# Kernel tuning notes

Hardware: AMD Instinct MI355X
Metric: run time of the kernel (lower is better)

The kernel has to match this reference:

```python
import jax, jax.numpy as jnp
import numpy as np
from jax import lax

B, C_IN, T = 256, 1, 1632
HID, CB_DIM, NUM_TOK, NUM_Q = 64, 512, 1024, 2


def conv_k2s2(x, W, b):
    # Conv1d(kernel=2, stride=2): x [B,Ci,T] -> [B,Co,T//2]; W [Co,Ci,2]
    Bx, Ci, Tx = x.shape
    xr = x.reshape(Bx, Ci, Tx // 2, 2)
    return jnp.einsum('bitk,oik->bot', xr, W) + b[None, :, None]


def convT_k2s2(x, W, b):
    # ConvTranspose1d(kernel=2, stride=2): x [B,Ci,T] -> [B,Co,2T]; W [Ci,Co,2] (torch layout)
    Bx, Ci, Tx = x.shape
    y = jnp.einsum('bit,iok->botk', x, W)  # [B,Co,T,2]
    Co = W.shape[1]
    return y.reshape(Bx, Co, 2 * Tx) + b[None, :, None]


def conv1x1(x, W, b):
    # W [Co,Ci]
    return jnp.einsum('bit,oi->bot', x, W) + b[None, :, None]


def residual_vq(x, codebooks):
    # x [B,t,D]; codebooks [NUM_Q, NUM_TOK, D]. Euclidean argmin + straight-through.
    residual = x
    quantized_out = jnp.zeros_like(x)
    all_idx, all_loss = [], []
    for q in range(codebooks.shape[0]):
        cb = codebooks[q]  # [N,D]
        # squared euclidean distance, single large GEMM
        d2 = (jnp.sum(residual ** 2, -1, keepdims=True)
              - 2.0 * jnp.einsum('btd,nd->btn', residual, cb)
              + jnp.sum(cb ** 2, -1))  # [B,t,N]
        idx = jnp.argmin(d2, axis=-1)  # [B,t]
        quant = cb[idx]  # gather [B,t,D]
        # commitment loss (codebook treated as fixed / EMA-updated)
        loss = jnp.mean((lax.stop_gradient(quant) - residual) ** 2)
        # straight-through estimator
        quant_st = residual + lax.stop_gradient(quant - residual)
        residual = residual - lax.stop_gradient(quant)
        quantized_out = quantized_out + quant_st
        all_idx.append(idx)
        all_loss.append(loss)
    return quantized_out, jnp.stack(all_idx, -1), jnp.stack(all_loss)


def setup_inputs() -> dict:
    key = jax.random.key(0)
    ks = jax.random.split(key, 16)
    s = 0.02
    return {
        'img': jax.random.normal(ks[0], (B, C_IN, T), jnp.float32),
        'W_e1': jax.random.normal(ks[1], (HID, C_IN, 2), jnp.float32) * s,
        'b_e1': jnp.zeros((HID,), jnp.float32),
        'W_e2': jax.random.normal(ks[2], (HID, HID, 2), jnp.float32) * s,
        'b_e2': jnp.zeros((HID,), jnp.float32),
        'W_e3': jax.random.normal(ks[3], (CB_DIM, HID), jnp.float32) * s,
        'b_e3': jnp.zeros((CB_DIM,), jnp.float32),
        'codebooks': jax.random.normal(ks[4], (NUM_Q, NUM_TOK, CB_DIM), jnp.float32),
        'Wt_d1': jax.random.normal(ks[5], (CB_DIM, HID, 2), jnp.float32) * s,
        'b_d1': jnp.zeros((HID,), jnp.float32),
        'Wt_d2': jax.random.normal(ks[6], (HID, HID, 2), jnp.float32) * s,
        'b_d2': jnp.zeros((HID,), jnp.float32),
        'W_d3': jax.random.normal(ks[7], (C_IN, HID), jnp.float32) * s,
        'b_d3': jnp.zeros((C_IN,), jnp.float32),
    }


def reference(img, W_e1, b_e1, W_e2, b_e2, W_e3, b_e3, codebooks,
              Wt_d1, b_d1, Wt_d2, b_d2, W_d3, b_d3):
    # encoder
    h = jax.nn.relu(conv_k2s2(img, W_e1, b_e1))
    h = jax.nn.relu(conv_k2s2(h, W_e2, b_e2))
    encoded = conv1x1(h, W_e3, b_e3)  # [B,512,408]
    # residual VQ over tokens
    x = jnp.transpose(encoded, (0, 2, 1))  # b c t -> b t c
    quantized, indices, commit_loss = residual_vq(x, codebooks)
    quantized = jnp.transpose(quantized, (0, 2, 1))  # b t c -> b c t
    # decoder
    d = jax.nn.relu(convT_k2s2(quantized, Wt_d1, b_d1))
    d = jax.nn.relu(convT_k2s2(d, Wt_d2, b_d2))
    out = conv1x1(d, W_d3, b_d3)  # [B,1,1632]
    recon_loss = jnp.mean((img - out) ** 2)
    return out, recon_loss, commit_loss, indices, quantized
```

## Files before the change

### kernel.cpp

```cpp
#include <hip/hip_runtime.h>

#define NB    256
#define TLEN  1632
#define HIDC  64
#define CBD   512
#define NTOK  1024
#define T2L   816
#define T4L   408
#define MTOK  (NB*T4L)
#define M2TOK (NB*T2L)
#define MOUT  (NB*TLEN)

#define DO_OUT    ((size_t)0)
#define DO_RECON  ((size_t)417792)
#define DO_IDX    ((size_t)417795)
#define DO_QUANT  ((size_t)626691)
#define DO_XRH    ((size_t)417796)
#define DO_R1H    (DO_XRH + (size_t)MTOK*256)

typedef unsigned short u16;
typedef unsigned long long u64;
typedef __attribute__((ext_vector_type(8))) short short8;
typedef __attribute__((ext_vector_type(4))) float f32x4;
typedef __attribute__((ext_vector_type(8))) _Float16 half8;
typedef __attribute__((ext_vector_type(4))) _Float16 half4;

static constexpr size_t OFF_XR  = 0;
static constexpr size_t OFF_H1  = OFF_XR + (size_t)MTOK*512;
static constexpr size_t OFF_H2  = OFF_H1 + (size_t)NB*T2L*64;
static constexpr size_t OFF_BE2 = OFF_H2 + (size_t)NB*T4L*64;
static constexpr size_t OFF_BD1 = OFF_BE2 + 8192;
static constexpr size_t OFF_BD2 = OFF_BD1 + 65536;
static constexpr size_t OFF_BX1 = OFF_BD2 + 8192;
static constexpr size_t OFF_BX2 = OFF_BX1 + 128;
static constexpr size_t OFF_ZB  = OFF_BX2 + 128;
static constexpr size_t OFF_C2  = OFF_ZB + 128;
static constexpr size_t OFF_SLOT= OFF_C2 + 2048;
static constexpr size_t OFF_IDXI= OFF_SLOT + 1536;
static constexpr size_t OFF_KEYS= OFF_IDXI + (size_t)MTOK*2;
static constexpr size_t OFF_FC  = OFF_KEYS + (size_t)MTOK*4;
static constexpr size_t OFF_FLAG= OFF_FC + 4;
static constexpr size_t OFF_CBH = OFF_FLAG + (size_t)MTOK*2;
static constexpr size_t OFF_CBL = OFF_CBH + 524288;
static constexpr size_t OFF_P0  = OFF_CBL + 524288;
static constexpr size_t OFF_P1  = OFF_P0 + 131072;
static constexpr size_t OFF_PAIRS = OFF_P1 + 131072;

__device__ inline u64 shfl_xor_u64_w16(u64 v, int m) {
    unsigned lo = (unsigned)v, hi = (unsigned)(v >> 32);
    lo = __shfl_xor(lo, m, 16);
    hi = __shfl_xor(hi, m, 16);
    return (((u64)hi) << 32) | lo;
}
__device__ inline u64 packkey(float d, int n) {
    unsigned u = __float_as_uint(d);
    u = (u & 0x80000000u) ? ~u : (u | 0x80000000u);
    return (((u64)u) << 32) | (unsigned)n;
}
__device__ inline float unpackd(u64 k) {
    unsigned u = (unsigned)(k >> 32);
    u = (u & 0x80000000u) ? (u & 0x7fffffffu) : ~u;
    return __uint_as_float(u);
}
__device__ inline void merge2(u64& k1, u64& k2, u64 o1, u64 o2) {
    u64 n1 = (k1 < o1) ? k1 : o1;
    u64 hi = (k1 < o1) ? o1 : k1;
    u64 cand = (k1 <= o1) ? k2 : o2;
    u64 n2 = (hi < cand) ? hi : cand;
    k1 = n1; k2 = n2;
}
__device__ inline half4 cvt_h4(float4 v) {
    half4 h;
    h.x = (_Float16)v.x; h.y = (_Float16)v.y;
    h.z = (_Float16)v.z; h.w = (_Float16)v.w;
    return h;
}
__device__ inline void gll16(const u16* g, u16* l) {
    __builtin_amdgcn_global_load_lds((const __attribute__((address_space(1))) void*)g,
                                     (__attribute__((address_space(3))) void*)l, 16, 0, 0);
}

__global__ void setup_kernel(const float* __restrict__ We2, const float* __restrict__ Wtd1,
                             const float* __restrict__ Wtd2, const float* __restrict__ bd1,
                             const float* __restrict__ bd2, const float* __restrict__ cbs,
                             float* __restrict__ Be2, float* __restrict__ Bd1,
                             float* __restrict__ Bd2, float* __restrict__ bx1, float* __restrict__ bx2,
                             u16* __restrict__ cbh, float* __restrict__ c2) {
    size_t t = (size_t)blockIdx.x * 256 + threadIdx.x;
    {
        float4 v = *(const float4*)(cbs + t * 4);
        *(half4*)&cbh[t * 4] = cvt_h4(v);
    }
    {
        int w = (int)(t >> 6);
        int lane = threadIdx.x & 63;
        if (w < 2048) {
            const float* r = cbs + (size_t)w * 512;
            float4 a = *(const float4*)(r + lane * 8);
            float4 b = *(const float4*)(r + lane * 8 + 4);
            float s = a.x*a.x + a.y*a.y + a.z*a.z + a.w*a.w + b.x*b.x + b.y*b.y + b.z*b.z + b.w*b.w;
            #pragma unroll
            for (int o = 32; o > 0; o >>= 1) s += __shfl_down(s, o, 64);
            if (lane == 0) c2[w] = s;
        }
    }
    size_t stride = (size_t)gridDim.x * 256;
    for (size_t x = t; x < 64 * 128; x += stride) {
        int c = (int)(x >> 7), k = (int)(x & 127);
        Be2[x] = We2[c * 128 + ((k & 63) << 1) + (k >> 6)];
    }
    for (size_t x = t; x < 128 * 512; x += stride) {
        int n = (int)(x >> 9), k = (int)(x & 511);
        Bd1[x] = Wtd1[k * 128 + n];
    }
    for (size_t x = t; x < 128 * 64; x += stride) {
        int n = (int)(x >> 6), k = (int)(x & 63);
        Bd2[x] = Wtd2[k * 128 + n];
    }
    for (size_t x = t; x < 128; x += stride) { bx1[x] = bd1[x >> 1]; bx2[x] = bd2[x >> 1]; }
}

__global__ void enc1_kernel(const float* __restrict__ img, const float* __restrict__ W,
                            const float* __restrict__ bias, float* __restrict__ h1) {
    int idx = blockIdx.x * 256 + threadIdx.x;
    int c = idx & 63;
    int t = (idx >> 6) % T2L;
    int b = idx / (64 * T2L);
    float v = W[c * 2] * img[(size_t)b * TLEN + 2 * t] +
              W[c * 2 + 1] * img[(size_t)b * TLEN + 2 * t + 1] + bias[c];
    h1[idx] = fmaxf(v, 0.f);
}

__global__ __launch_bounds__(256) void gemm_nt(const float* __restrict__ A, const float* __restrict__ Bw,
                        const float* __restrict__ bias, float* __restrict__ C,
                        int M, int N, int K, int amode, int relu, u16* __restrict__ xh) {
    __shared__ float As[32][132];
    __shared__ float Bs[32][68];
    int m0 = blockIdx.x * 128;
    int n0 = blockIdx.y * 64;
    int tid = threadIdx.x;
    int tx = tid & 15;
    int ty = tid >> 4;
    float acc[8][4];
    #pragma unroll
    for (int i = 0; i < 8; ++i)
        #pragma unroll
        for (int j = 0; j < 4; ++j) acc[i][j] = 0.f;

    for (int k0 = 0; k0 < K; k0 += 32) {
        #pragma unroll
        for (int i = 0; i < 4; ++i) {
            int idx = tid + i * 256;
            int row = idx >> 3;
            int kq = idx & 7;
            int m = m0 + row;
            size_t base;
            if (amode == 0) base = (size_t)m * K;
            else            base = (size_t)(((m / T4L) * T2L + 2 * (m % T4L)) * 64);
            float4 v = *(const float4*)(A + base + k0 + kq * 4);
            int kk = kq * 4;
            As[kk + 0][row] = v.x; As[kk + 1][row] = v.y;
            As[kk + 2][row] = v.z; As[kk + 3][row] = v.w;
        }
        #pragma unroll
        for (int i = 0; i < 2; ++i) {
            int idx = tid + i * 256;
            int row = idx >> 3;
            int kq = idx & 7;
            float4 v = *(const float4*)(Bw + (size_t)(n0 + row) * K + k0 + kq * 4);
            int kk = kq * 4;
            Bs[kk + 0][row] = v.x; Bs[kk + 1][row] = v.y;
            Bs[kk + 2][row] = v.z; Bs[kk + 3][row] = v.w;
        }
        __syncthreads();
        #pragma unroll
        for (int kk = 0; kk < 32; ++kk) {
            float a[8], bf[4];
            float4 a0 = *(const float4*)&As[kk][ty * 8];
            float4 a1 = *(const float4*)&As[kk][ty * 8 + 4];
            a[0]=a0.x; a[1]=a0.y; a[2]=a0.z; a[3]=a0.w;
            a[4]=a1.x; a[5]=a1.y; a[6]=a1.z; a[7]=a1.w;
            float4 b0 = *(const float4*)&Bs[kk][tx * 4];
            bf[0]=b0.x; bf[1]=b0.y; bf[2]=b0.z; bf[3]=b0.w;
            #pragma unroll
            for (int i = 0; i < 8; ++i)
                #pragma unroll
                for (int j = 0; j < 4; ++j) acc[i][j] += a[i] * bf[j];
        }
        __syncthreads();
    }
    #pragma unroll
    for (int i = 0; i < 8; ++i) {
        int m = m0 + ty * 8 + i;
        float4 v;
        v.x = acc[i][0] + bias[n0 + tx * 4 + 0];
        v.y = acc[i][1] + bias[n0 + tx * 4 + 1];
        v.z = acc[i][2] + bias[n0 + tx * 4 + 2];
        v.w = acc[i][3] + bias[n0 + tx * 4 + 3];
        if (relu) { v.x=fmaxf(v.x,0.f); v.y=fmaxf(v.y,0.f); v.z=fmaxf(v.z,0.f); v.w=fmaxf(v.w,0.f); }
        *(float4*)(C + (size_t)m * N + n0 + tx * 4) = v;
        if (xh) *(half4*)&xh[(size_t)m * N + n0 + tx * 4] = cvt_h4(v);
    }
}

__global__ void r1_prep(const u16* __restrict__ xrh, const u16* __restrict__ cbh0,
                        const u64* __restrict__ keys, u16* __restrict__ r1h) {
    int m = blockIdx.x * 8 + (threadIdx.x >> 5);
    int l = threadIdx.x & 31;
    int i0 = (int)(keys[m] & 0xFFFFFFFFull);
    const half8* xp = (const half8*)(xrh + (size_t)m * 512 + l * 16);
    const half8* cp = (const half8*)(cbh0 + (size_t)i0 * 512 + l * 16);
    half8* rp = (half8*)(r1h + (size_t)m * 512 + l * 16);
    rp[0] = xp[0] - cp[0];
    rp[1] = xp[1] - cp[1];
}

__global__ __launch_bounds__(256, 2) void vq_f16_gll(
    const u16* __restrict__ Ah, const u16* __restrict__ cbh,
    const float* __restrict__ c2, u64* __restrict__ pairs)
{
    __shared__ __align__(16) u16 As[2][128 * 32];
    __shared__ __align__(16) u16 Bs[2][256 * 32];
    int tid = threadIdx.x;
    int n0 = blockIdx.x * 256, m0 = blockIdx.y * 128;
    int lane = tid & 63, wid = tid >> 6;
    int lm = lane & 15, quad = lane >> 4;
    int wm = wid >> 1, wn = wid & 1;

    f32x4 acc[4][8];
    #pragma unroll
    for (int i = 0; i < 4; ++i)
        #pragma unroll
        for (int j = 0; j < 8; ++j) acc[i][j] = (f32x4){0.f, 0.f, 0.f, 0.f};

    int arow[2], achk[2];
    #pragma unroll
    for (int i = 0; i < 2; ++i) {
        int slot = wid * 128 + i * 64 + lane;
        arow[i] = slot >> 2;
        achk[i] = (slot & 3) ^ ((arow[i] >> 1) & 3);
    }
    int brow[4], bchk[4];
    #pragma unroll
    for (int i = 0; i < 4; ++i) {
        brow[i] = i * 64 + wid * 16 + (lane >> 2);
        bchk[i] = (lane & 3) ^ ((brow[i] >> 1) & 3);
    }

#define VQ_GLL(BUF, K0)                                                               \
    {                                                                                 \
        _Pragma("unroll")                                                             \
        for (int i = 0; i < 2; ++i)                                                   \
            gll16(Ah + (size_t)(m0 + arow[i]) * 512 + (K0) + achk[i] * 8,             \
                  &As[BUF][wid * 1024 + i * 512]);                                    \
        _Pragma("unroll")                                                             \
        for (int i = 0; i < 4; ++i)                                                   \
            gll16(cbh + (size_t)(n0 + brow[i]) * 512 + (K0) + bchk[i] * 8,            \
                  &Bs[BUF][i * 2048 + wid * 512]);                                    \
    }

#define VQ_COMPUTE(BUF) {                                                             \
        half8 ah[4];                                                                  \
        _Pragma("unroll")                                                             \
        for (int mt = 0; mt < 4; ++mt) {                                              \
            int r = wm * 64 + mt * 16 + lm;                                           \
            ah[mt] = *(const half8*)&As[BUF][r * 32 + ((quad ^ ((r >> 1) & 3)) * 8)]; \
        }                                                                             \
        _Pragma("unroll")                                                             \
        for (int nt = 0; nt < 8; ++nt) {                                              \
            int rn = wn * 128 + nt * 16 + lm;                                         \
            half8 bh = *(const half8*)&Bs[BUF][rn * 32 + ((quad ^ ((rn >> 1) & 3)) * 8)]; \
            _Pragma("unroll")                                                         \
            for (int mt = 0; mt < 4; ++mt)                                            \
                acc[mt][nt] = __builtin_amdgcn_mfma_f32_16x16x32_f16(ah[mt], bh, acc[mt][nt], 0, 0, 0); \
        }                                                                             \
    }

    VQ_GLL(0, 0);
    __syncthreads();
    for (int t = 0; t < 16; ++t) {
        int buf = t & 1;
        if (t < 15) VQ_GLL(buf ^ 1, (t + 1) * 32);
        VQ_COMPUTE(buf);
        __syncthreads();
    }
#undef VQ_GLL
#undef VQ_COMPUTE

    float c2v[8];
    #pragma unroll
    for (int nt = 0; nt < 8; ++nt) c2v[nt] = c2[n0 + wn * 128 + nt * 16 + lm];

    u64* scr = (u64*)&As[0][0];
    #pragma unroll
    for (int mt = 0; mt < 4; ++mt) {
        #pragma unroll
        for (int rg = 0; rg < 4; ++rg) {
            int tl = wm * 64 + mt * 16 + quad * 4 + rg;
            u64 k1 = ~0ull, k2 = ~0ull;
            #pragma unroll
            for (int nt = 0; nt < 8; ++nt) {
                float d = c2v[nt] - 2.0f * acc[mt][nt][rg];
                u64 k = packkey(d, n0 + wn * 128 + nt * 16 + lm);
                if (k < k1) { k2 = k1; k1 = k; } else if (k < k2) { k2 = k; }
            }
            #pragma unroll
            for (int s = 1; s < 16; s <<= 1) {
                u64 o1 = shfl_xor_u64_w16(k1, s);
                u64 o2 = shfl_xor_u64_w16(k2, s);
                merge2(k1, k2, o1, o2);
            }
            if (lm == 0) { scr[wn * 256 + tl * 2] = k1; scr[wn * 256 + tl * 2 + 1] = k2; }
        }
    }
    __syncthreads();
    if (tid < 128) {
        u64 a1 = scr[tid * 2], a2 = scr[tid * 2 + 1];
        merge2(a1, a2, scr[256 + tid * 2], scr[256 + tid * 2 + 1]);
        size_t base = (size_t)(m0 + tid) * 8 + blockIdx.x * 2;
        pairs[base] = a1; pairs[base + 1] = a2;
    }
}

__global__ void vq_reduce(const u64* __restrict__ pairs, u64* __restrict__ keybuf,
                          int* __restrict__ fc, int* __restrict__ flaglist, float tau) {
    int m = blockIdx.x * 256 + threadIdx.x;
    const u64* p = pairs + (size_t)m * 8;
    u64 k1 = ~0ull, k2 = ~0ull;
    #pragma unroll
    for (int i = 0; i < 8; ++i) {
        u64 k = p[i];
        if (k < k1) { k2 = k1; k1 = k; } else if (k < k2) { k2 = k; }
    }
    keybuf[m] = k1;
    if (unpackd(k2) - unpackd(k1) < tau) {
        int pos = atomicAdd(fc, 1);
        flaglist[pos] = m;
    }
}

__global__ void vq_rescue(const float* __restrict__ xr, const float* __restrict__ cb,
                          const float* __restrict__ c2, const float* __restrict__ cb0,
                          const u64* __restrict__ prevkeys,
                          const int* __restrict__ fc, const int* __restrict__ flaglist,
                          u64* __restrict__ keybuf) {
    __shared__ u64 red[4];
    int cnt = *fc;
    int lane = threadIdx.x & 63, wid = threadIdx.x >> 6;
    for (int f = blockIdx.x; f < cnt; f += gridDim.x) {
        int m = flaglist[f];
        float4 rv0 = *(const float4*)(xr + (size_t)m * 512 + lane * 8);
        float4 rv1 = *(const float4*)(xr + (size_t)m * 512 + lane * 8 + 4);
        if (cb0) {
            size_t co = (size_t)(prevkeys[m] & 0xFFFFFFFFull) * 512;
            float4 c0 = *(const float4*)(cb0 + co + lane * 8);
            float4 c1 = *(const float4*)(cb0 + co + lane * 8 + 4);
            rv0.x -= c0.x; rv0.y -= c0.y; rv0.z -= c0.z; rv0.w -= c0.w;
            rv1.x -= c1.x; rv1.y -= c1.y; rv1.z -= c1.z; rv1.w -= c1.w;
        }
        u64 best = ~0ull;
        for (int c = wid * 256; c < wid * 256 + 256; ++c) {
            const float* cp = cb + (size_t)c * 512 + lane * 8;
            float4 c0 = *(const float4*)cp;
            float4 c1 = *(const float4*)(cp + 4);
            float p = rv0.x*c0.x + rv0.y*c0.y + rv0.z*c0.z + rv0.w*c0.w
                    + rv1.x*c1.x + rv1.y*c1.y + rv1.z*c1.z + rv1.w*c1.w;
            #pragma unroll
            for (int s = 1; s < 64; s <<= 1) p += __shfl_xor(p, s, 64);
            u64 k = packkey(c2[c] - 2.0f * p, c);
            if (k < best) best = k;
        }
        if (lane == 0) red[wid] = best;
        __syncthreads();
        if (threadIdx.x == 0) {
            u64 b = red[0];
            if (red[1] < b) b = red[1];
            if (red[2] < b) b = red[2];
            if (red[3] < b) b = red[3];
            keybuf[m] = b;
        }
        __syncthreads();
    }
}

__global__ void commit_idx_kernel(const float* __restrict__ xr,
                                  const float* __restrict__ cb0f, const float* __restrict__ cb1f,
                                  const u64* __restrict__ keys0, const u64* __restrict__ keys1,
                                  float* __restrict__ idx_f, int* __restrict__ idx_i,
                                  float* __restrict__ slots) {
    int tid = threadIdx.x;
    int lane = tid & 63;
    int m = blockIdx.x * 4 + (tid >> 6);
    unsigned i0 = (unsigned)(keys0[m] & 0xFFFFFFFFull);
    unsigned i1 = (unsigned)(keys1[m] & 0xFFFFFFFFull);
    const float* x = xr + (size_t)m * 512 + lane * 8;
    const float* c0 = cb0f + (size_t)i0 * 512 + lane * 8;
    const float* c1 = cb1f + (size_t)i1 * 512 + lane * 8;
    float4 x0 = *(const float4*)x, x1 = *(const float4*)(x + 4);
    float4 a0 = *(const float4*)c0, a1 = *(const float4*)(c0 + 4);
    float4 b0 = *(const float4*)c1, b1 = *(const float4*)(c1 + 4);
    x0.x -= a0.x; x0.y -= a0.y; x0.z -= a0.z; x0.w -= a0.w;
    x1.x -= a1.x; x1.y -= a1.y; x1.z -= a1.z; x1.w -= a1.w;
    float s1 = x0.x*x0.x + x0.y*x0.y + x0.z*x0.z + x0.w*x0.w
             + x1.x*x1.x + x1.y*x1.y + x1.z*x1.z + x1.w*x1.w;
    x0.x -= b0.x; x0.y -= b0.y; x0.z -= b0.z; x0.w -= b0.w;
    x1.x -= b1.x; x1.y -= b1.y; x1.z -= b1.z; x1.w -= b1.w;
    float s2 = x0.x*x0.x + x0.y*x0.y + x0.z*x0.z + x0.w*x0.w
             + x1.x*x1.x + x1.y*x1.y + x1.z*x1.z + x1.w*x1.w;
    #pragma unroll
    for (int o = 32; o > 0; o >>= 1) { s1 += __shfl_down(s1, o, 64); s2 += __shfl_down(s2, o, 64); }
    if (lane == 0) {
        atomicAdd(&slots[512 + (m & 511)], s1);
        atomicAdd(&slots[1024 + (m & 511)], s2);
        idx_f[(size_t)m * 2]     = (float)i0;
        idx_f[(size_t)m * 2 + 1] = (float)i1;
        idx_i[m * 2] = (int)i0;
        idx_i[m * 2 + 1] = (int)i1;
    }
}

__global__ void quant_out_kernel(const float* __restrict__ cb0, const float* __restrict__ cb1,
                                 const int* __restrict__ idxi, float* __restrict__ out4) {
    __shared__ float buf[64][129];
    __shared__ int i0s[64], i1s[64];
    int b = blockIdx.x;
    int t0 = blockIdx.y * 64;
    int c0 = blockIdx.z * 128;
    int tid = threadIdx.x;
    if (tid < 64) {
        int t = t0 + tid;
        int i0 = 0, i1 = 0;
        if (t < T4L) { i0 = idxi[(b * T4L + t) * 2]; i1 = idxi[(b * T4L + t) * 2 + 1]; }
        i0s[tid] = i0; i1s[tid] = i1;
    }
    __syncthreads();
    int cl = tid & 127, th = tid >> 7;
    for (int t = th; t < 64; t += 2) {
        if (t0 + t < T4L)
            buf[t][cl] = cb0[(size_t)i0s[t] * 512 + c0 + cl] + cb1[(size_t)i1s[t] * 512 + c0 + cl];
    }
    __syncthreads();
    int lane = tid & 63, ch = tid >> 6;
    for (int cc = ch; cc < 128; cc += 4) {
        int t = t0 + lane;
        if (t < T4L) out4[((size_t)b * 512 + c0 + cc) * T4L + t] = buf[lane][cc];
    }
}

__global__ void d1_gather_kernel(const float* __restrict__ P0, const float* __restrict__ P1,
                                 const int* __restrict__ idxi, const float* __restrict__ bx1,
                                 float* __restrict__ d1) {
    int x = blockIdx.x * 256 + threadIdx.x;
    int n = x & 127;
    int m = x >> 7;
    int b = m / T4L, t = m % T4L;
    int i0 = idxi[m * 2], i1 = idxi[m * 2 + 1];
    float v = P0[i0 * 128 + n] + P1[i1 * 128 + n] + bx1[n];
    v = fmaxf(v, 0.f);
    d1[((size_t)(b * T2L + 2 * t + (n & 1))) * 64 + (n >> 1)] = v;
}

__global__ __launch_bounds__(256) void dec2_fused(
    const float* __restrict__ d1, const float* __restrict__ Bd2, const float* __restrict__ bx2,
    const float* __restrict__ W3, const float* __restrict__ b3, const float* __restrict__ img,
    float* __restrict__ out, float* __restrict__ slots)
{
    __shared__ float As[32][132];
    __shared__ float Bs[32][132];
    __shared__ float w3s[64];
    int m0 = blockIdx.x * 128;
    int tid = threadIdx.x;
    int tx = tid & 15;
    int ty = tid >> 4;
    if (tid < 64) w3s[tid] = W3[tid];
    float acc[8][8];
    #pragma unroll
    for (int i = 0; i < 8; ++i)
        #pragma unroll
        for (int j = 0; j < 8; ++j) acc[i][j] = 0.f;

    for (int k0 = 0; k0 < 64; k0 += 32) {
        #pragma unroll
        for (int i = 0; i < 4; ++i) {
            int idx = tid + i * 256;
            int row = idx >> 3;
            int kq = idx & 7;
            float4 v = *(const float4*)(d1 + (size_t)(m0 + row) * 64 + k0 + kq * 4);
            int kk = kq * 4;
            As[kk + 0][row] = v.x; As[kk + 1][row] = v.y;
            As[kk + 2][row] = v.z; As[kk + 3][row] = v.w;
        }
        #pragma unroll
        for (int i = 0; i < 4; ++i) {
            int idx = tid + i * 256;
            int row = idx >> 3;
            int kq = idx & 7;
            float4 v = *(const float4*)(Bd2 + (size_t)row * 64 + k0 + kq * 4);
            int kk = kq * 4;
            Bs[kk + 0][row] = v.x; Bs[kk + 1][row] = v.y;
            Bs[kk + 2][row] = v.z; Bs[kk + 3][row] = v.w;
        }
        __syncthreads();
        #pragma unroll
        for (int kk = 0; kk < 32; ++kk) {
            float a[8], bf[8];
            float4 a0 = *(const float4*)&As[kk][ty * 8];
            float4 a1 = *(const float4*)&As[kk][ty * 8 + 4];
            a[0]=a0.x; a[1]=a0.y; a[2]=a0.z; a[3]=a0.w;
            a[4]=a1.x; a[5]=a1.y; a[6]=a1.z; a[7]=a1.w;
            float4 b0 = *(const float4*)&Bs[kk][tx * 4];
            float4 b1 = *(const float4*)&Bs[kk][64 + tx * 4];
            bf[0]=b0.x; bf[1]=b0.y; bf[2]=b0.z; bf[3]=b0.w;
            bf[4]=b1.x; bf[5]=b1.y; bf[6]=b1.z; bf[7]=b1.w;
            #pragma unroll
            for (int i = 0; i < 8; ++i)
                #pragma unroll
                for (int j = 0; j < 8; ++j) acc[i][j] += a[i] * bf[j];
        }
        __syncthreads();
    }
    float bb3 = b3[0];
    float local = 0.f;
    #pragma unroll
    for (int i = 0; i < 8; ++i) {
        float s0 = 0.f, s1 = 0.f;
        #pragma unroll
        for (int j = 0; j < 4; ++j) {
            int n = tx * 4 + j;
            float v = fmaxf(acc[i][j] + bx2[n], 0.f);
            float w = w3s[n >> 1];
            if (j & 1) s1 += w * v; else s0 += w * v;
            int n2 = 64 + tx * 4 + j;
            float v2 = fmaxf(acc[i][j + 4] + bx2[n2], 0.f);
            float w2 = w3s[n2 >> 1];
            if (j & 1) s1 += w2 * v2; else s0 += w2 * v2;
        }
        #pragma unroll
        for (int o = 8; o > 0; o >>= 1) { s0 += __shfl_down(s0, o, 16); s1 += __shfl_down(s1, o, 16); }
        if (tx == 0) {
            int m = m0 + ty * 8 + i;
            int b = m / T2L, t2 = m % T2L;
            size_t o0 = (size_t)b * TLEN + 2 * t2;
            float v0 = s0 + bb3, v1 = s1 + bb3;
            out[o0] = v0; out[o0 + 1] = v1;
            float e0 = img[o0] - v0, e1 = img[o0 + 1] - v1;
            local += e0 * e0 + e1 * e1;
        }
    }
    if (tx == 0) atomicAdd(&slots[(blockIdx.x * 16 + ty) & 511], local);
}

__global__ void finalize_kernel(const float* __restrict__ slots, float* __restrict__ out_scalars) {
    __shared__ float red[256];
    int tid = threadIdx.x;
    for (int which = 0; which < 3; ++which) {
        float s = slots[which * 512 + tid] + slots[which * 512 + tid + 256];
        red[tid] = s; __syncthreads();
        for (int st = 128; st > 0; st >>= 1) { if (tid < st) red[tid] += red[tid + st]; __syncthreads(); }
        if (tid == 0) {
            float denom = (which == 0) ? (float)MOUT : (float)((size_t)MTOK * 512);
            out_scalars[which] = red[0] / denom;
        }
        __syncthreads();
    }
}

extern "C" void kernel_launch(void* const* d_in, const int* in_sizes, int n_in,
                              void* d_out, int out_size, void* d_ws, size_t ws_size,
                              hipStream_t stream) {
    const float* img  = (const float*)d_in[0];
    const float* We1  = (const float*)d_in[1];
    const float* be1  = (const float*)d_in[2];
    const float* We2  = (const float*)d_in[3];
    const float* be2  = (const float*)d_in[4];
    const float* We3  = (const float*)d_in[5];
    const float* be3  = (const float*)d_in[6];
    const float* cbs  = (const float*)d_in[7];
    const float* Wtd1 = (const float*)d_in[8];
    const float* bd1  = (const float*)d_in[9];
    const float* Wtd2 = (const float*)d_in[10];
    const float* bd2  = (const float*)d_in[11];
    const float* Wd3  = (const float*)d_in[12];
    const float* bd3  = (const float*)d_in[13];

    float* w = (float*)d_ws;
    float* xr   = w + OFF_XR;
    float* h1   = w + OFF_H1;
    float* h2   = w + OFF_H2;
    float* Be2  = w + OFF_BE2;
    float* Bd1  = w + OFF_BD1;
    float* Bd2  = w + OFF_BD2;
    float* bx1  = w + OFF_BX1;
    float* bx2  = w + OFF_BX2;
    float* zerob= w + OFF_ZB;
    float* c2   = w + OFF_C2;
    float* slots= w + OFF_SLOT;
    int*   idxi = (int*)(w + OFF_IDXI);
    u64*   keys = (u64*)(w + OFF_KEYS);
    int*   fc   = (int*)(w + OFF_FC);
    int*   flag = (int*)(w + OFF_FLAG);
    u16*   cbh  = (u16*)(w + OFF_CBH);
    float* P0   = w + OFF_P0;
    float* P1   = w + OFF_P1;
    u64*   pairs= (u64*)(w + OFF_PAIRS);

    float* outp = (float*)d_out;
    float* out0   = outp + DO_OUT;
    float* oscal  = outp + DO_RECON;
    float* idxf   = outp + DO_IDX;
    float* qout   = outp + DO_QUANT;
    u16*   xrh    = (u16*)(outp + DO_XRH);
    u16*   r1h    = (u16*)(outp + DO_R1H);

    hipMemsetAsync(slots, 0, 1536 * sizeof(float), stream);
    hipMemsetAsync(fc, 0, 2 * sizeof(int), stream);
    hipMemsetAsync(zerob, 0, 128 * sizeof(float), stream);

    setup_kernel<<<1024, 256, 0, stream>>>(We2, Wtd1, Wtd2, bd1, bd2, cbs,
                                           Be2, Bd1, Bd2, bx1, bx2, cbh, c2);

    const float* cb1p = cbs + (size_t)NTOK * CBD;

    gemm_nt<<<dim3(8, 2), 256, 0, stream>>>(cbs,  Bd1, zerob, P0, 1024, 128, 512, 0, 0, nullptr);
    gemm_nt<<<dim3(8, 2), 256, 0, stream>>>(cb1p, Bd1, zerob, P1, 1024, 128, 512, 0, 0, nullptr);

    enc1_kernel<<<(NB * T2L * HIDC) / 256, 256, 0, stream>>>(img, We1, be1, h1);
    gemm_nt<<<dim3(MTOK / 128, 1), 256, 0, stream>>>(h1, Be2, be2, h2, MTOK, 64, 128, 1, 1, nullptr);
    gemm_nt<<<dim3(MTOK / 128, 8), 256, 0, stream>>>(h2, We3, be3, xr, MTOK, 512, 64, 0, 0, xrh);

    vq_f16_gll<<<dim3(4, MTOK / 128), 256, 0, stream>>>(xrh, cbh, c2, pairs);
    vq_reduce<<<MTOK / 256, 256, 0, stream>>>(pairs, keys, fc + 0, flag, 0.05f);
    vq_rescue<<<1024, 256, 0, stream>>>(xr, cbs, c2, nullptr, nullptr, fc + 0, flag, keys);
    r1_prep<<<MTOK / 8, 256, 0, stream>>>(xrh, cbh, keys, r1h);
    vq_f16_gll<<<dim3(4, MTOK / 128), 256, 0, stream>>>(r1h, cbh + (size_t)NTOK * 512, c2 + NTOK, pairs);
    vq_reduce<<<MTOK / 256, 256, 0, stream>>>(pairs, keys + MTOK, fc + 1, flag + MTOK, 0.15f);
    vq_rescue<<<1024, 256, 0, stream>>>(xr, cb1p, c2 + NTOK, cbs, keys, fc + 1, flag + MTOK, keys + MTOK);

    commit_idx_kernel<<<MTOK / 4, 256, 0, stream>>>(xr, cbs, cb1p, keys, keys + MTOK, idxf, idxi, slots);

    quant_out_kernel<<<dim3(NB, 7, 4), 256, 0, stream>>>(cbs, cb1p, idxi, qout);

    d1_gather_kernel<<<(MTOK * 128) / 256, 256, 0, stream>>>(P0, P1, idxi, bx1, h1);
    dec2_fused<<<M2TOK / 128, 256, 0, stream>>>(h1, Bd2, bx2, Wd3, bd3, img, out0, slots);

    finalize_kernel<<<1, 256, 0, stream>>>(slots, oscal);
}
```

Baseline: 1.239 ms.

## Enlarge VQ GEMM tile to 256x256 with 512 threads and 4-stage LDS pipeline

The VQ distance GEMM kernel now uses 512-thread blocks covering 256 tokens by 256 codes, up from 128 by 256. Its two-buffer LDS loop with a full __syncthreads per step becomes a four-buffer ring that prefetches two k-steps ahead, using explicit vmcnt waits and raw s_barrier. The aim is to halve codebook reloads per token and hide global-load latency better. In exchange LDS use grows to 128 KB per block, which limits occupancy. Reuse of a buffer two steps later relies on the barrier ordering being exactly right.

Result: faster. 1.155 ms (-6.8%).

```diff
diff --git a/kernel.cpp b/kernel.cpp
--- a/kernel.cpp
+++ b/kernel.cpp
@@ -215,14 +215,14 @@
     rp[1] = xp[1] - cp[1];
 }
 
-__global__ __launch_bounds__(256, 2) void vq_f16_gll(
+__global__ __launch_bounds__(512, 2) void vq_f16_gll(
     const u16* __restrict__ Ah, const u16* __restrict__ cbh,
     const float* __restrict__ c2, u64* __restrict__ pairs)
 {
-    __shared__ __align__(16) u16 As[2][128 * 32];
-    __shared__ __align__(16) u16 Bs[2][256 * 32];
+    __shared__ __align__(16) u16 As[4][256 * 32];
+    __shared__ __align__(16) u16 Bs[4][256 * 32];
     int tid = threadIdx.x;
-    int n0 = blockIdx.x * 256, m0 = blockIdx.y * 128;
+    int n0 = blockIdx.x * 256, m0 = blockIdx.y * 256;
     int lane = tid & 63, wid = tid >> 6;
     int lm = lane & 15, quad = lane >> 4;
     int wm = wid >> 1, wn = wid & 1;
@@ -233,30 +233,22 @@
         #pragma unroll
         for (int j = 0; j < 8; ++j) acc[i][j] = (f32x4){0.f, 0.f, 0.f, 0.f};
 
-    int arow[2], achk[2];
+    int srow[2], schk[2];
     #pragma unroll
     for (int i = 0; i < 2; ++i) {
-        int slot = wid * 128 + i * 64 + lane;
-        arow[i] = slot >> 2;
-        achk[i] = (slot & 3) ^ ((arow[i] >> 1) & 3);
-    }
-    int brow[4], bchk[4];
-    #pragma unroll
-    for (int i = 0; i < 4; ++i) {
-        brow[i] = i * 64 + wid * 16 + (lane >> 2);
-        bchk[i] = (lane & 3) ^ ((brow[i] >> 1) & 3);
+        int s = wid + i * 8;
+        srow[i] = s * 16 + (lane >> 2);
+        schk[i] = (lane & 3) ^ ((srow[i] >> 1) & 3);
     }
 
 #define VQ_GLL(BUF, K0)                                                               \
-    {                                                                                 \
-        _Pragma("unroll")                                                             \
-        for (int i = 0; i < 2; ++i)                                                   \
-            gll16(Ah + (size_t)(m0 + arow[i]) * 512 + (K0) + achk[i] * 8,             \
-                  &As[BUF][wid * 1024 + i * 512]);                                    \
-        _Pragma("unroll")                                                             \
-        for (int i = 0; i < 4; ++i)                                                   \
-            gll16(cbh + (size_t)(n0 + brow[i]) * 512 + (K0) + bchk[i] * 8,            \
-                  &Bs[BUF][i * 2048 + wid * 512]);                                    \
+    _Pragma("unroll")                                                                 \
+    for (int i = 0; i < 2; ++i) {                                                     \
+        int s = wid + i * 8;                                                          \
+        gll16(Ah + (size_t)(m0 + srow[i]) * 512 + (K0) + schk[i] * 8,                 \
+              &As[BUF][s * 512]);                                                     \
+        gll16(cbh + (size_t)(n0 + srow[i]) * 512 + (K0) + schk[i] * 8,                \
+              &Bs[BUF][s * 512]);                                                     \
     }
 
 #define VQ_COMPUTE(BUF) {                                                             \
@@ -277,12 +269,16 @@
     }
 
     VQ_GLL(0, 0);
-    __syncthreads();
+    VQ_GLL(1, 32);
+    #pragma unroll
     for (int t = 0; t < 16; ++t) {
-        int buf = t & 1;
-        if (t < 15) VQ_GLL(buf ^ 1, (t + 1) * 32);
-        VQ_COMPUTE(buf);
-        __syncthreads();
+        if (t + 2 < 16) VQ_GLL((t + 2) & 3, (t + 2) * 32);
+        if (t <= 13)      asm volatile("s_waitcnt vmcnt(8)" ::: "memory");
+        else if (t == 14) asm volatile("s_waitcnt vmcnt(4)" ::: "memory");
+        else              asm volatile("s_waitcnt vmcnt(0)" ::: "memory");
+        __builtin_amdgcn_s_barrier();
+        __builtin_amdgcn_sched_barrier(0);
+        VQ_COMPUTE(t & 3);
     }
 #undef VQ_GLL
 #undef VQ_COMPUTE
@@ -310,13 +306,13 @@
                 u64 o2 = shfl_xor_u64_w16(k2, s);
                 merge2(k1, k2, o1, o2);
             }
-            if (lm == 0) { scr[wn * 256 + tl * 2] = k1; scr[wn * 256 + tl * 2 + 1] = k2; }
+            if (lm == 0) { scr[wn * 512 + tl * 2] = k1; scr[wn * 512 + tl * 2 + 1] = k2; }
         }
     }
     __syncthreads();
-    if (tid < 128) {
+    if (tid < 256) {
         u64 a1 = scr[tid * 2], a2 = scr[tid * 2 + 1];
-        merge2(a1, a2, scr[256 + tid * 2], scr[256 + tid * 2 + 1]);
+        merge2(a1, a2, scr[512 + tid * 2], scr[512 + tid * 2 + 1]);
         size_t base = (size_t)(m0 + tid) * 8 + blockIdx.x * 2;
         pairs[base] = a1; pairs[base + 1] = a2;
     }
@@ -628,11 +624,11 @@
     gemm_nt<<<dim3(MTOK / 128, 1), 256, 0, stream>>>(h1, Be2, be2, h2, MTOK, 64, 128, 1, 1, nullptr);
     gemm_nt<<<dim3(MTOK / 128, 8), 256, 0, stream>>>(h2, We3, be3, xr, MTOK, 512, 64, 0, 0, xrh);
 
-    vq_f16_gll<<<dim3(4, MTOK / 128), 256, 0, stream>>>(xrh, cbh, c2, pairs);
+    vq_f16_gll<<<dim3(4, MTOK / 256), 512, 0, stream>>>(xrh, cbh, c2, pairs);
     vq_reduce<<<MTOK / 256, 256, 0, stream>>>(pairs, keys, fc + 0, flag, 0.05f);
     vq_rescue<<<1024, 256, 0, stream>>>(xr, cbs, c2, nullptr, nullptr, fc + 0, flag, keys);
     r1_prep<<<MTOK / 8, 256, 0, stream>>>(xrh, cbh, keys, r1h);
-    vq_f16_gll<<<dim3(4, MTOK / 128), 256, 0, stream>>>(r1h, cbh + (size_t)NTOK * 512, c2 + NTOK, pairs);
+    vq_f16_gll<<<dim3(4, MTOK / 256), 512, 0, stream>>>(r1h, cbh + (size_t)NTOK * 512, c2 + NTOK, pairs);
     vq_reduce<<<MTOK / 256, 256, 0, stream>>>(pairs, keys + MTOK, fc + 1, flag + MTOK, 0.15f);
     vq_rescue<<<1024, 256, 0, stream>>>(xr, cb1p, c2 + NTOK, cbs, keys, fc + 1, flag + MTOK, keys + MTOK);
 
```
